# Kernel tuning notes

Measured on AMD Instinct MI355X. Metric: run time of the kernel, lower is better.

## Reference

```python
import jax, jax.numpy as jnp
import numpy as np

BATCH = 16384
D = 4096  # input_features


def setup_inputs() -> dict:
    key = jax.random.key(0)
    k1, k2, k3 = jax.random.split(key, 3)
    x0 = jax.random.normal(k1, (BATCH, D), dtype=jnp.float32)
    x_cross = jax.random.normal(k2, (BATCH, D), dtype=jnp.float32)
    # RandomNormal(mean=0, stddev=sqrt(2/input_features))
    w = jax.random.normal(k3, (D,), dtype=jnp.float32) * np.float32(np.sqrt(2.0 / D))
    b = jnp.full((D,), 0.1, dtype=jnp.float32)
    return {"x0": x0, "x_cross": x_cross, "w": w, "b": b}


def reference(x0, x_cross, w, b):
    # Original: tensordot(x0[:, :, None] @ x_cross[:, None, :], w, [[-1],[0]]) + b + x_cross
    # Algebraically identical fused form (avoids the O(B*d^2) intermediate):
    #   x0 * (x_cross . w) + b + x_cross
    s = jnp.einsum("bd,d->b", x_cross, w)  # [B]
    return x0 * s[:, None] + b + x_cross
```

## Files before the change

### kernel.cpp

```cpp
#include <hip/hip_runtime.h>


typedef float f32x4 __attribute__((ext_vector_type(4)));

constexpr int D_DIM = 4096;
constexpr int TPB   = 256;
constexpr int V4    = D_DIM / 4;
constexpr int F4PT  = V4 / TPB;

__global__ __launch_bounds__(TPB)
void cross_fused_kernel(const float* __restrict__ x0,
                        const float* __restrict__ xc,
                        const float* __restrict__ w,
                        const float* __restrict__ bias,
                        float* __restrict__ out) {
    const int row = blockIdx.x;
    const size_t base = (size_t)row * D_DIM;

    const f32x4* __restrict__ xc4  = (const f32x4*)(xc + base);
    const f32x4* __restrict__ x04  = (const f32x4*)(x0 + base);
    const f32x4* __restrict__ w4   = (const f32x4*)w;
    const f32x4* __restrict__ b4   = (const f32x4*)bias;
    f32x4* __restrict__       out4 = (f32x4*)(out + base);

    const int t = threadIdx.x;

    f32x4 xcv[F4PT];
    f32x4 x0v[F4PT];
#pragma unroll
    for (int i = 0; i < F4PT; ++i) {
        const int idx = t + i * TPB;
        xcv[i] = xc4[idx];
        x0v[i] = x04[idx];
    }

    float partial = 0.0f;
#pragma unroll
    for (int i = 0; i < F4PT; ++i) {
        const int idx = t + i * TPB;
        const f32x4 wv = w4[idx];
        partial += xcv[i].x * wv.x + xcv[i].y * wv.y
                 + xcv[i].z * wv.z + xcv[i].w * wv.w;
    }

#pragma unroll
    for (int off = 32; off >= 1; off >>= 1)
        partial += __shfl_down(partial, off);

    __shared__ float wsum[TPB / 64];
    const int lane = t & 63, wid = t >> 6;
    if (lane == 0) wsum[wid] = partial;
    __syncthreads();
    const float s = wsum[0] + wsum[1] + wsum[2] + wsum[3];

#pragma unroll
    for (int i = 0; i < F4PT; ++i) {
        const int idx = t + i * TPB;
        const f32x4 bv = b4[idx];
        f32x4 o;
        o.x = fmaf(x0v[i].x, s, bv.x + xcv[i].x);
        o.y = fmaf(x0v[i].y, s, bv.y + xcv[i].y);
        o.z = fmaf(x0v[i].z, s, bv.z + xcv[i].z);
        o.w = fmaf(x0v[i].w, s, bv.w + xcv[i].w);
        __builtin_nontemporal_store(o, &out4[idx]);
    }
}

extern "C" void kernel_launch(void* const* d_in, const int* in_sizes, int n_in,
                              void* d_out, int out_size, void* d_ws, size_t ws_size,
                              hipStream_t stream) {
    const float* x0   = (const float*)d_in[0];
    const float* xc   = (const float*)d_in[1];
    const float* w    = (const float*)d_in[2];
    const float* bias = (const float*)d_in[3];
    float* out        = (float*)d_out;

    const int rows = in_sizes[0] / D_DIM;
    cross_fused_kernel<<<rows, TPB, 0, stream>>>(x0, xc, w, bias, out);
}
```

Baseline: 138.4 us.

## Map one row per wavefront and defer x0 loads until after reduction

Each 64-lane wavefront now owns a whole row, so a block processes four rows and the shared-memory reduction and __syncthreads barrier go away; the dot product uses a shfl_xor butterfly with four independent accumulators. The x0 loads move into the output loop after the reduction, which cuts register pressure (xc only, 16 float4 per lane) but serializes x0 traffic behind the dot product. The grid shrinks by four, and each lane now loads 16 float4 of xc plus w instead of 4.

```diff
diff --git a/kernel.cpp b/kernel.cpp
--- a/kernel.cpp
+++ b/kernel.cpp
@@ -5,8 +5,9 @@
 
 constexpr int D_DIM = 4096;
 constexpr int TPB   = 256;
-constexpr int V4    = D_DIM / 4;
-constexpr int F4PT  = V4 / TPB;
+constexpr int ROWS_PER_BLOCK = TPB / 64;
+constexpr int V4_ROW = D_DIM / 4;
+constexpr int F4PL   = V4_ROW / 64;
 
 __global__ __launch_bounds__(TPB)
 void cross_fused_kernel(const float* __restrict__ x0,
@@ -14,7 +15,9 @@
                         const float* __restrict__ w,
                         const float* __restrict__ bias,
                         float* __restrict__ out) {
-    const int row = blockIdx.x;
+    const int wid  = threadIdx.x >> 6;
+    const int lane = threadIdx.x & 63;
+    const int row  = blockIdx.x * ROWS_PER_BLOCK + wid;
     const size_t base = (size_t)row * D_DIM;
 
     const f32x4* __restrict__ xc4  = (const f32x4*)(xc + base);
@@ -23,45 +26,37 @@
     const f32x4* __restrict__ b4   = (const f32x4*)bias;
     f32x4* __restrict__       out4 = (f32x4*)(out + base);
 
-    const int t = threadIdx.x;
+    f32x4 xcv[F4PL];
+#pragma unroll
+    for (int i = 0; i < F4PL; ++i)
+        xcv[i] = xc4[lane + 64 * i];
 
-    f32x4 xcv[F4PT];
-    f32x4 x0v[F4PT];
+    float p0 = 0.f, p1 = 0.f, p2 = 0.f, p3 = 0.f;
 #pragma unroll
-    for (int i = 0; i < F4PT; ++i) {
-        const int idx = t + i * TPB;
-        xcv[i] = xc4[idx];
-        x0v[i] = x04[idx];
+    for (int i = 0; i < F4PL; ++i) {
+        const f32x4 wv = w4[lane + 64 * i];
+        p0 += xcv[i].x * wv.x;
+        p1 += xcv[i].y * wv.y;
+        p2 += xcv[i].z * wv.z;
+        p3 += xcv[i].w * wv.w;
     }
-
-    float partial = 0.0f;
-#pragma unroll
-    for (int i = 0; i < F4PT; ++i) {
-        const int idx = t + i * TPB;
-        const f32x4 wv = w4[idx];
-        partial += xcv[i].x * wv.x + xcv[i].y * wv.y
-                 + xcv[i].z * wv.z + xcv[i].w * wv.w;
-    }
+    float partial = (p0 + p1) + (p2 + p3);
 
 #pragma unroll
     for (int off = 32; off >= 1; off >>= 1)
-        partial += __shfl_down(partial, off);
+        partial += __shfl_xor(partial, off);
+    const float s = partial;
 
-    __shared__ float wsum[TPB / 64];
-    const int lane = t & 63, wid = t >> 6;
-    if (lane == 0) wsum[wid] = partial;
-    __syncthreads();
-    const float s = wsum[0] + wsum[1] + wsum[2] + wsum[3];
-
-#pragma unroll
-    for (int i = 0; i < F4PT; ++i) {
-        const int idx = t + i * TPB;
-        const f32x4 bv = b4[idx];
+#pragma unroll 4
+    for (int i = 0; i < F4PL; ++i) {
+        const int idx = lane + 64 * i;
+        const f32x4 x0v = x04[idx];
+        const f32x4 bv  = b4[idx];
         f32x4 o;
-        o.x = fmaf(x0v[i].x, s, bv.x + xcv[i].x);
-        o.y = fmaf(x0v[i].y, s, bv.y + xcv[i].y);
-        o.z = fmaf(x0v[i].z, s, bv.z + xcv[i].z);
-        o.w = fmaf(x0v[i].w, s, bv.w + xcv[i].w);
+        o.x = fmaf(x0v.x, s, bv.x + xcv[i].x);
+        o.y = fmaf(x0v.y, s, bv.y + xcv[i].y);
+        o.z = fmaf(x0v.z, s, bv.z + xcv[i].z);
+        o.w = fmaf(x0v.w, s, bv.w + xcv[i].w);
         __builtin_nontemporal_store(o, &out4[idx]);
     }
 }
@@ -76,5 +71,5 @@
     float* out        = (float*)d_out;
 
     const int rows = in_sizes[0] / D_DIM;
-    cross_fused_kernel<<<rows, TPB, 0, stream>>>(x0, xc, w, bias, out);
+    cross_fused_kernel<<<rows / ROWS_PER_BLOCK, TPB, 0, stream>>>(x0, xc, w, bias, out);
 }
```

Result: slower. 204.9 us (+48.0%).

## Split fused row kernel into dot-product kernel and grid-stride elementwise kernel

Applied to the files above, without the earlier changes.

Replaces the single per-row fused kernel with two launches: one computes the per-row dot product of x_cross with w into a workspace buffer, the other applies x0*s + b + x_cross with a grid-stride loop. The intent is to shorten each block's dependency chain and let the elementwise pass stream freely without a block-wide barrier. In exchange, x_cross is read from global memory twice and a second launch is added, which raises total memory traffic for a bandwidth-bound operation.

```diff
diff --git a/kernel.cpp b/kernel.cpp
--- a/kernel.cpp
+++ b/kernel.cpp
@@ -9,60 +9,65 @@
 constexpr int F4PT  = V4 / TPB;
 
 __global__ __launch_bounds__(TPB)
-void cross_fused_kernel(const float* __restrict__ x0,
-                        const float* __restrict__ xc,
-                        const float* __restrict__ w,
-                        const float* __restrict__ bias,
-                        float* __restrict__ out) {
+void cross_dot_kernel(const float* __restrict__ xc,
+                      const float* __restrict__ w,
+                      float* __restrict__ s_out) {
     const int row = blockIdx.x;
     const size_t base = (size_t)row * D_DIM;
-
-    const f32x4* __restrict__ xc4  = (const f32x4*)(xc + base);
-    const f32x4* __restrict__ x04  = (const f32x4*)(x0 + base);
-    const f32x4* __restrict__ w4   = (const f32x4*)w;
-    const f32x4* __restrict__ b4   = (const f32x4*)bias;
-    f32x4* __restrict__       out4 = (f32x4*)(out + base);
+    const f32x4* __restrict__ xc4 = (const f32x4*)(xc + base);
+    const f32x4* __restrict__ w4  = (const f32x4*)w;
 
     const int t = threadIdx.x;
 
-    f32x4 xcv[F4PT];
-    f32x4 x0v[F4PT];
+    float p0 = 0.f, p1 = 0.f, p2 = 0.f, p3 = 0.f;
 #pragma unroll
     for (int i = 0; i < F4PT; ++i) {
         const int idx = t + i * TPB;
-        xcv[i] = xc4[idx];
-        x0v[i] = x04[idx];
+        const f32x4 xcv = xc4[idx];
+        const f32x4 wv  = w4[idx];
+        p0 += xcv.x * wv.x;
+        p1 += xcv.y * wv.y;
+        p2 += xcv.z * wv.z;
+        p3 += xcv.w * wv.w;
     }
-
-    float partial = 0.0f;
-#pragma unroll
-    for (int i = 0; i < F4PT; ++i) {
-        const int idx = t + i * TPB;
-        const f32x4 wv = w4[idx];
-        partial += xcv[i].x * wv.x + xcv[i].y * wv.y
-                 + xcv[i].z * wv.z + xcv[i].w * wv.w;
-    }
+    float partial = (p0 + p1) + (p2 + p3);
 
 #pragma unroll
     for (int off = 32; off >= 1; off >>= 1)
-        partial += __shfl_down(partial, off);
+        partial += __shfl_xor(partial, off);
 
     __shared__ float wsum[TPB / 64];
     const int lane = t & 63, wid = t >> 6;
     if (lane == 0) wsum[wid] = partial;
     __syncthreads();
-    const float s = wsum[0] + wsum[1] + wsum[2] + wsum[3];
+    if (t == 0)
+        s_out[row] = wsum[0] + wsum[1] + wsum[2] + wsum[3];
+}
 
-#pragma unroll
-    for (int i = 0; i < F4PT; ++i) {
-        const int idx = t + i * TPB;
-        const f32x4 bv = b4[idx];
+__global__ __launch_bounds__(TPB)
+void cross_ew_kernel(const float* __restrict__ x0,
+                     const float* __restrict__ xc,
+                     const float* __restrict__ s_in,
+                     const float* __restrict__ bias,
+                     float* __restrict__ out,
+                     long total4) {
+    const f32x4* __restrict__ x04 = (const f32x4*)x0;
+    const f32x4* __restrict__ xc4 = (const f32x4*)xc;
+    const f32x4* __restrict__ b4  = (const f32x4*)bias;
+    f32x4* __restrict__       o4  = (f32x4*)out;
+
+    const long stride = (long)gridDim.x * TPB;
+    for (long i4 = (long)blockIdx.x * TPB + threadIdx.x; i4 < total4; i4 += stride) {
+        const f32x4 xcv = xc4[i4];
+        const f32x4 x0v = __builtin_nontemporal_load(&x04[i4]);
+        const float s   = s_in[i4 >> 10];
+        const f32x4 bv  = b4[i4 & (V4 - 1)];
         f32x4 o;
-        o.x = fmaf(x0v[i].x, s, bv.x + xcv[i].x);
-        o.y = fmaf(x0v[i].y, s, bv.y + xcv[i].y);
-        o.z = fmaf(x0v[i].z, s, bv.z + xcv[i].z);
-        o.w = fmaf(x0v[i].w, s, bv.w + xcv[i].w);
-        __builtin_nontemporal_store(o, &out4[idx]);
+        o.x = fmaf(x0v.x, s, bv.x + xcv.x);
+        o.y = fmaf(x0v.y, s, bv.y + xcv.y);
+        o.z = fmaf(x0v.z, s, bv.z + xcv.z);
+        o.w = fmaf(x0v.w, s, bv.w + xcv.w);
+        __builtin_nontemporal_store(o, &o4[i4]);
     }
 }
 
@@ -74,7 +79,11 @@
     const float* w    = (const float*)d_in[2];
     const float* bias = (const float*)d_in[3];
     float* out        = (float*)d_out;
+    float* s_buf      = (float*)d_ws;
 
     const int rows = in_sizes[0] / D_DIM;
-    cross_fused_kernel<<<rows, TPB, 0, stream>>>(x0, xc, w, bias, out);
+    const long total4 = (long)rows * V4;
+
+    cross_dot_kernel<<<rows, TPB, 0, stream>>>(xc, w, s_buf);
+    cross_ew_kernel<<<2048, TPB, 0, stream>>>(x0, xc, s_buf, bias, out, total4);
 }
```

New measurement: 166.9 us. 1.21x slower.
